# Optimization experiments

Hardware: AMD Instinct MI355X
Metric: run time of the kernel (lower is better)

## Reference

```python
import jax, jax.numpy as jnp
import numpy as np

N = 100000      # nodes_num
E = 1600000     # edges (avg degree 16)
D_IN = 256
D_OUT = 128
EPS = 1e-3      # keras BatchNormalization default epsilon
LEAKY = 0.2     # tf.nn.leaky_relu default alpha


def setup_inputs() -> dict:
    key = jax.random.key(0)
    ks = jax.random.split(key, 6)
    x = jax.random.normal(ks[0], (N, D_IN), jnp.float32)
    w = jax.random.normal(ks[1], (D_IN, D_OUT), jnp.float32) / np.float32(np.sqrt(D_IN))
    w1 = jax.random.normal(ks[2], (D_IN, D_IN), jnp.float32) / np.float32(np.sqrt(D_IN))
    w2 = jax.random.normal(ks[3], (D_IN, D_IN), jnp.float32) / np.float32(np.sqrt(D_IN))
    rows = jnp.sort(jax.random.randint(ks[4], (E,), 0, N, jnp.int32))
    cols = jax.random.randint(ks[5], (E,), 0, N, jnp.int32)
    edge_vals = jnp.ones((E,), jnp.float32)
    return {"x": x, "w": w, "w1": w1, "w2": w2,
            "edge_vals": edge_vals, "rows": rows, "cols": cols}


def reference(x, w, w1, w2, edge_vals, rows, cols):
    # Batch norm (training mode: per-feature stats over node axis, gamma=1, beta=0)
    mean = jnp.mean(x, axis=0)
    var = jnp.var(x, axis=0)
    xn = (x - mean) * jax.lax.rsqrt(var + EPS)          # [N, D_IN]

    mapped = xn @ w                                      # [N, D_OUT]
    s1 = jnp.tanh(jnp.sum((xn @ w1) * xn, axis=1))       # [N] row score
    s2 = jnp.tanh(jnp.sum((xn @ w2) * xn, axis=1))       # [N] col score

    # sparse add of adj*s1[row] and adj*s2[col], then leaky_relu on edge values
    ev = edge_vals * (s1[rows] + s2[cols])               # [E]
    ev = jnp.where(ev > 0, ev, LEAKY * ev)

    # tf.sparse.softmax: softmax over the nonzero entries of each row
    m = jax.ops.segment_max(ev, rows, num_segments=N)    # [N]
    m = jnp.where(jnp.isfinite(m), m, 0.0)               # empty rows -> 0
    ex = jnp.exp(ev - m[rows])
    denom = jax.ops.segment_sum(ex, rows, num_segments=N)
    alpha = ex / denom[rows]                             # [E] edge softmax

    # SpMM: out[i] = sum_{e: rows[e]==i} alpha[e] * mapped[cols[e]]
    out = jax.ops.segment_sum(alpha[:, None] * mapped[cols], rows, num_segments=N)
    return out  # activation is identity (activation=None)
```

## Files before the change

### kernel.cpp

```cpp
#include <hip/hip_runtime.h>

#define D_IN 256
#define D_OUT 128
#define EPS_BN 1e-3f
#define LEAKY 0.2f

typedef unsigned short u16;
typedef unsigned int u32;
typedef u16 u16x4 __attribute__((ext_vector_type(4)));
typedef u16 u16x8 __attribute__((ext_vector_type(8)));
typedef __bf16 bf16x8 __attribute__((ext_vector_type(8)));
typedef float f32x4 __attribute__((ext_vector_type(4)));

__device__ __forceinline__ float bf2f(u16 u) {
    u32 v = ((u32)u) << 16;
    return __uint_as_float(v);
}
__device__ __forceinline__ u16 f2bf(float f) {
    u32 u = __float_as_uint(f);
    u32 r = (u + 0x7FFFu + ((u >> 16) & 1u)) >> 16;
    return (u16)r;
}

__global__ void colstats_k(const float* __restrict__ x, int n,
                           float* __restrict__ sums, float* __restrict__ sqs) {
    int c = threadIdx.x;
    float s = 0.f, q = 0.f;
    for (int r = blockIdx.x; r < n; r += gridDim.x) {
        float v = x[(size_t)r * D_IN + c];
        s += v;
        q += v * v;
    }
    atomicAdd(&sums[c], s);
    atomicAdd(&sqs[c], q);
}

__global__ void finalize_k(const float* __restrict__ sums, const float* __restrict__ sqs,
                           int n, float* __restrict__ mean, float* __restrict__ inv) {
    int c = threadIdx.x;
    float m = sums[c] / (float)n;
    float v = sqs[c] / (float)n - m * m;
    mean[c] = m;
    inv[c] = rsqrtf(v + EPS_BN);
}

__global__ void prep_w_k(const float* __restrict__ w1, const float* __restrict__ w2,
                         const float* __restrict__ w, u16* __restrict__ Bth,
                         u16* __restrict__ Btl, u16* __restrict__ Wth,
                         u16* __restrict__ Wtl) {
    int idx = blockIdx.x * 256 + threadIdx.x;
    int k = idx & 255;
    int nn = idx >> 8;
    if (nn < 512) {
        float v = (nn < 256) ? w1[(size_t)k * 256 + nn]
                             : w2[(size_t)k * 256 + (nn - 256)];
        u16 h = f2bf(v);
        u16 l = f2bf(v - bf2f(h));
        Bth[(size_t)nn * 256 + k] = h;
        Btl[(size_t)nn * 256 + k] = l;
    } else {
        int nm = nn - 512;
        float v = w[(size_t)k * D_OUT + nm];
        u16 h = f2bf(v);
        u16 l = f2bf(v - bf2f(h));
        Wth[(size_t)nm * 256 + k] = h;
        Wtl[(size_t)nm * 256 + k] = l;
    }
}

__device__ __forceinline__ int kmap(int v, int g, int j) {
    return (v == 0) ? (8 * g + j) : (16 * (j >> 2) + 4 * g + (j & 3));
}

__global__ void probe_k(int* __restrict__ flagp) {
    __shared__ float Ar[16][32];
    __shared__ float Br[32][16];
    __shared__ float Dr[16][16];
    int l = threadIdx.x;
    for (int i = l; i < 512; i += 64) {
        int r = i >> 5, k = i & 31;
        Ar[r][k] = (float)(((r * 5 + k * 3) % 11) - 5);
    }
    for (int i = l; i < 512; i += 64) {
        int k = i >> 4, c = i & 15;
        Br[k][c] = (float)(((k * 3 + c * 7) % 13) - 6);
    }
    __syncthreads();
    for (int i = l; i < 256; i += 64) {
        int r = i >> 4, c = i & 15;
        float s = 0.f;
        for (int k = 0; k < 32; ++k) s += Ar[r][k] * Br[k][c];
        Dr[r][c] = s;
    }
    __syncthreads();
    int g = l >> 4, c15 = l & 15;
    int found = -1;
    for (int combo = 0; combo < 4; ++combo) {
        int va = combo >> 1, vb = combo & 1;
        u16x8 af, bfv;
#pragma unroll
        for (int j = 0; j < 8; ++j) {
            af[j] = f2bf(Ar[c15][kmap(va, g, j)]);
            bfv[j] = f2bf(Br[kmap(vb, g, j)][c15]);
        }
        f32x4 d = {0.f, 0.f, 0.f, 0.f};
        d = __builtin_amdgcn_mfma_f32_16x16x32_bf16(
            __builtin_bit_cast(bf16x8, af), __builtin_bit_cast(bf16x8, bfv), d,
            0, 0, 0);
        bool ok = true;
#pragma unroll
        for (int r = 0; r < 4; ++r) ok = ok && (d[r] == Dr[g * 4 + r][c15]);
        if (found < 0 && __all(ok)) found = combo;
    }
    if (l == 0) flagp[0] = (found < 0) ? 0 : found;
}

__device__ __forceinline__ void stage_A(const float* __restrict__ x,
                                        const float* __restrict__ mean,
                                        const float* __restrict__ inv, int m0,
                                        int n, u16* Ah, u16* Al) {
    const int tid = threadIdx.x;
    for (int i = 0; i < 16; ++i) {
        int chunk = tid + (i << 8);
        int r = chunk >> 6;
        int c4 = (chunk & 63) << 2;
        int gr = m0 + r;
        bool ok = gr < n;
        float4 v = make_float4(0.f, 0.f, 0.f, 0.f);
        if (ok) v = *(const float4*)(x + (size_t)gr * D_IN + c4);
        float4 mn = *(const float4*)(mean + c4);
        float4 iv = *(const float4*)(inv + c4);
        float a0 = ok ? (v.x - mn.x) * iv.x : 0.f;
        float a1 = ok ? (v.y - mn.y) * iv.y : 0.f;
        float a2 = ok ? (v.z - mn.z) * iv.z : 0.f;
        float a3 = ok ? (v.w - mn.w) * iv.w : 0.f;
        u16 h0 = f2bf(a0), h1 = f2bf(a1), h2 = f2bf(a2), h3 = f2bf(a3);
        u16 l0 = f2bf(a0 - bf2f(h0)), l1 = f2bf(a1 - bf2f(h1));
        u16 l2 = f2bf(a2 - bf2f(h2)), l3 = f2bf(a3 - bf2f(h3));
        int off = (r << 9) + (((c4 << 1) ^ ((r & 7) << 4)));
        u16x4 hv = {h0, h1, h2, h3};
        u16x4 lv = {l0, l1, l2, l3};
        *(u16x4*)((char*)Ah + off) = hv;
        *(u16x4*)((char*)Al + off) = lv;
    }
}

__device__ __forceinline__ void stage_B(const u16* __restrict__ Gh,
                                        const u16* __restrict__ Gl, int n0,
                                        int k0, u16* Bh, u16* Bl) {
    const int tid = threadIdx.x;
    for (int i = 0; i < 2; ++i) {
        int chunk = tid + (i << 8);
        int nl = chunk >> 3;
        int k8 = (chunk & 7) << 3;
        size_t goff = (size_t)(n0 + nl) * 256 + k0 + k8;
        u16x8 hv = *(const u16x8*)(Gh + goff);
        u16x8 lv = *(const u16x8*)(Gl + goff);
        int off = (nl << 7) + (((k8 << 1) ^ ((nl & 7) << 4)));
        *(u16x8*)((char*)Bh + off) = hv;
        *(u16x8*)((char*)Bl + off) = lv;
    }
}

template <int V>
__device__ __forceinline__ bf16x8 ld_frag(const u16* plane, int rowByteBase,
                                          int swz, int kbyte, int g) {
    const char* p = (const char*)plane + rowByteBase;
    if constexpr (V == 0) {
        u16x8 v = *(const u16x8*)(p + ((kbyte + (g << 4)) ^ swz));
        return __builtin_bit_cast(bf16x8, v);
    } else {
        u16x4 a = *(const u16x4*)(p + ((kbyte + (g << 3)) ^ swz));
        u16x4 b = *(const u16x4*)(p + ((kbyte + 32 + (g << 3)) ^ swz));
        u16x8 v;
        v[0] = a[0]; v[1] = a[1]; v[2] = a[2]; v[3] = a[3];
        v[4] = b[0]; v[5] = b[1]; v[6] = b[2]; v[7] = b[3];
        return __builtin_bit_cast(bf16x8, v);
    }
}

template <int VA, int VB>
__device__ __forceinline__ void quadmap_body(
    const float* __restrict__ x, const u16* __restrict__ Bth,
    const u16* __restrict__ Btl, const u16* __restrict__ Wth,
    const u16* __restrict__ Wtl, const float* __restrict__ mean,
    const float* __restrict__ inv, float* __restrict__ s1,
    float* __restrict__ s2, u16* __restrict__ mapped, int n, int mapCT,
    u16* Ah, u16* Al, u16* Bh, u16* Bl) {
    const int tid = threadIdx.x;
    const int lane = tid & 63, wave = tid >> 6;
    const int g = lane >> 4, c15 = lane & 15;
    const int wm = wave >> 1, wn = wave & 1;
    const int m0 = blockIdx.x * 64;

    stage_A(x, mean, inv, m0, n, Ah, Al);
    __syncthreads();

    float sp[2][4] = {{0.f, 0.f, 0.f, 0.f}, {0.f, 0.f, 0.f, 0.f}};

    for (int jt = 0; jt < 8; ++jt) {
        f32x4 acc[2][2];
#pragma unroll
        for (int mf = 0; mf < 2; ++mf)
#pragma unroll
            for (int nf = 0; nf < 2; ++nf) acc[mf][nf] = (f32x4){0.f, 0.f, 0.f, 0.f};

        for (int kt = 0; kt < 4; ++kt) {
            __syncthreads();
            stage_B(Bth, Btl, jt * 64, kt * 64, Bh, Bl);
            __syncthreads();
#pragma unroll
            for (int kk = 0; kk < 2; ++kk) {
                int kbA = kt * 128 + kk * 64;
                int kbB = kk * 64;
                bf16x8 ah[2], alf[2], bhf[2], blf[2];
#pragma unroll
                for (int mf = 0; mf < 2; ++mf) {
                    int row = wm * 32 + mf * 16 + c15;
                    int swz = (row & 7) << 4;
                    ah[mf] = ld_frag<VA>(Ah, row << 9, swz, kbA, g);
                    alf[mf] = ld_frag<VA>(Al, row << 9, swz, kbA, g);
                }
#pragma unroll
                for (int nf = 0; nf < 2; ++nf) {
                    int nl = wn * 32 + nf * 16 + c15;
                    int swz = (nl & 7) << 4;
                    bhf[nf] = ld_frag<VB>(Bh, nl << 7, swz, kbB, g);
                    blf[nf] = ld_frag<VB>(Bl, nl << 7, swz, kbB, g);
                }
#pragma unroll
                for (int mf = 0; mf < 2; ++mf)
#pragma unroll
                    for (int nf = 0; nf < 2; ++nf) {
                        acc[mf][nf] = __builtin_amdgcn_mfma_f32_16x16x32_bf16(
                            ah[mf], bhf[nf], acc[mf][nf], 0, 0, 0);
                        acc[mf][nf] = __builtin_amdgcn_mfma_f32_16x16x32_bf16(
                            ah[mf], blf[nf], acc[mf][nf], 0, 0, 0);
                        acc[mf][nf] = __builtin_amdgcn_mfma_f32_16x16x32_bf16(
                            alf[mf], bhf[nf], acc[mf][nf], 0, 0, 0);
                    }
            }
        }
        int fcol0 = (jt & 3) << 6;
#pragma unroll
        for (int mf = 0; mf < 2; ++mf) {
#pragma unroll
            for (int nf = 0; nf < 2; ++nf) {
                int col = fcol0 + wn * 32 + nf * 16 + c15;
                float mn = mean[col], ivv = inv[col];
#pragma unroll
                for (int r = 0; r < 4; ++r) {
                    int grow = m0 + wm * 32 + mf * 16 + g * 4 + r;
                    float xv = 0.f;
                    if (grow < n) xv = (x[(size_t)grow * D_IN + col] - mn) * ivv;
                    sp[mf][r] = fmaf(acc[mf][nf][r], xv, sp[mf][r]);
                }
            }
        }
        if ((jt & 3) == 3) {
            float part[2][4];
#pragma unroll
            for (int mf = 0; mf < 2; ++mf)
#pragma unroll
                for (int r = 0; r < 4; ++r) {
                    float v = sp[mf][r];
                    v += __shfl_xor(v, 1);
                    v += __shfl_xor(v, 2);
                    v += __shfl_xor(v, 4);
                    v += __shfl_xor(v, 8);
                    part[mf][r] = v;
                    sp[mf][r] = 0.f;
                }
            float* scratch = (float*)Bh;
            __syncthreads();
            if (c15 == 0) {
#pragma unroll
                for (int mf = 0; mf < 2; ++mf)
#pragma unroll
                    for (int r = 0; r < 4; ++r) {
                        int sidx = (((((wm << 2) | g) << 1) | mf) << 3) | (r << 1) | wn;
                        scratch[sidx] = part[mf][r];
                    }
            }
            __syncthreads();
            if (wn == 0 && c15 == 0) {
                float* dst = (jt < 4) ? s1 : s2;
#pragma unroll
                for (int mf = 0; mf < 2; ++mf)
#pragma unroll
                    for (int r = 0; r < 4; ++r) {
                        int sidx = (((((wm << 2) | g) << 1) | mf) << 3) | (r << 1);
                        float tot = scratch[sidx] + scratch[sidx | 1];
                        int grow = m0 + wm * 32 + mf * 16 + g * 4 + r;
                        if (grow < n) dst[grow] = tanhf(tot);
                    }
            }
            __syncthreads();
        }
    }

    const int tiles = mapCT >> 6;
    for (int t = 0; t < tiles; ++t) {
        f32x4 acc[2][2];
#pragma unroll
        for (int mf = 0; mf < 2; ++mf)
#pragma unroll
            for (int nf = 0; nf < 2; ++nf) acc[mf][nf] = (f32x4){0.f, 0.f, 0.f, 0.f};

        for (int kt = 0; kt < 4; ++kt) {
            __syncthreads();
            stage_B(Wth, Wtl, t * 64, kt * 64, Bh, Bl);
            __syncthreads();
#pragma unroll
            for (int kk = 0; kk < 2; ++kk) {
                int kbA = kt * 128 + kk * 64;
                int kbB = kk * 64;
                bf16x8 ah[2], alf[2], bhf[2], blf[2];
#pragma unroll
                for (int mf = 0; mf < 2; ++mf) {
                    int row = wm * 32 + mf * 16 + c15;
                    int swz = (row & 7) << 4;
                    ah[mf] = ld_frag<VA>(Ah, row << 9, swz, kbA, g);
                    alf[mf] = ld_frag<VA>(Al, row << 9, swz, kbA, g);
                }
#pragma unroll
                for (int nf = 0; nf < 2; ++nf) {
                    int nl = wn * 32 + nf * 16 + c15;
                    int swz = (nl & 7) << 4;
                    bhf[nf] = ld_frag<VB>(Bh, nl << 7, swz, kbB, g);
                    blf[nf] = ld_frag<VB>(Bl, nl << 7, swz, kbB, g);
                }
#pragma unroll
                for (int mf = 0; mf < 2; ++mf)
#pragma unroll
                    for (int nf = 0; nf < 2; ++nf) {
                        acc[mf][nf] = __builtin_amdgcn_mfma_f32_16x16x32_bf16(
                            ah[mf], bhf[nf], acc[mf][nf], 0, 0, 0);
                        acc[mf][nf] = __builtin_amdgcn_mfma_f32_16x16x32_bf16(
                            ah[mf], blf[nf], acc[mf][nf], 0, 0, 0);
                        acc[mf][nf] = __builtin_amdgcn_mfma_f32_16x16x32_bf16(
                            alf[mf], bhf[nf], acc[mf][nf], 0, 0, 0);
                    }
            }
        }
#pragma unroll
        for (int mf = 0; mf < 2; ++mf)
#pragma unroll
            for (int nf = 0; nf < 2; ++nf) {
                int si = t * 64 + wn * 32 + nf * 16 + c15;
#pragma unroll
                for (int r = 0; r < 4; ++r) {
                    int grow = m0 + wm * 32 + mf * 16 + g * 4 + r;
                    if (grow < n)
                        mapped[(size_t)grow * mapCT + si] = f2bf(acc[mf][nf][r]);
                }
            }
    }
}

__global__ __launch_bounds__(256) void quadmap_mfma_k(
    const float* __restrict__ x, const u16* __restrict__ Bth,
    const u16* __restrict__ Btl, const u16* __restrict__ Wth,
    const u16* __restrict__ Wtl, const float* __restrict__ mean,
    const float* __restrict__ inv, float* __restrict__ s1,
    float* __restrict__ s2, u16* __restrict__ mapped,
    const int* __restrict__ flagp, int n, int mapCT) {
    __shared__ u16 Ah[64 * 256];
    __shared__ u16 Al[64 * 256];
    __shared__ u16 Bh[64 * 64];
    __shared__ u16 Bl[64 * 64];
    int v = flagp[0];
    if (v == 1)
        quadmap_body<0, 1>(x, Bth, Btl, Wth, Wtl, mean, inv, s1, s2, mapped, n, mapCT, Ah, Al, Bh, Bl);
    else if (v == 2)
        quadmap_body<1, 0>(x, Bth, Btl, Wth, Wtl, mean, inv, s1, s2, mapped, n, mapCT, Ah, Al, Bh, Bl);
    else if (v == 3)
        quadmap_body<1, 1>(x, Bth, Btl, Wth, Wtl, mean, inv, s1, s2, mapped, n, mapCT, Ah, Al, Bh, Bl);
    else
        quadmap_body<0, 0>(x, Bth, Btl, Wth, Wtl, mean, inv, s1, s2, mapped, n, mapCT, Ah, Al, Bh, Bl);
}

template <int VA, int VB>
__device__ __forceinline__ void map_body(
    const float* __restrict__ x, const u16* __restrict__ Wth,
    const u16* __restrict__ Wtl, const float* __restrict__ mean,
    const float* __restrict__ inv, u16* __restrict__ mapped, int n, int c0,
    int CT, u16* Ah, u16* Al, u16* Bh, u16* Bl) {
    const int tid = threadIdx.x;
    const int lane = tid & 63, wave = tid >> 6;
    const int g = lane >> 4, c15 = lane & 15;
    const int wm = wave >> 1, wn = wave & 1;
    const int m0 = blockIdx.x * 64;

    stage_A(x, mean, inv, m0, n, Ah, Al);
    __syncthreads();

    const int tiles = CT >> 6;
    for (int t = 0; t < tiles; ++t) {
        f32x4 acc[2][2];
#pragma unroll
        for (int mf = 0; mf < 2; ++mf)
#pragma unroll
            for (int nf = 0; nf < 2; ++nf) acc[mf][nf] = (f32x4){0.f, 0.f, 0.f, 0.f};

        for (int kt = 0; kt < 4; ++kt) {
            __syncthreads();
            stage_B(Wth, Wtl, c0 + t * 64, kt * 64, Bh, Bl);
            __syncthreads();
#pragma unroll
            for (int kk = 0; kk < 2; ++kk) {
                int kbA = kt * 128 + kk * 64;
                int kbB = kk * 64;
                bf16x8 ah[2], alf[2], bhf[2], blf[2];
#pragma unroll
                for (int mf = 0; mf < 2; ++mf) {
                    int row = wm * 32 + mf * 16 + c15;
                    int swz = (row & 7) << 4;
                    ah[mf] = ld_frag<VA>(Ah, row << 9, swz, kbA, g);
                    alf[mf] = ld_frag<VA>(Al, row << 9, swz, kbA, g);
                }
#pragma unroll
                for (int nf = 0; nf < 2; ++nf) {
                    int nl = wn * 32 + nf * 16 + c15;
                    int swz = (nl & 7) << 4;
                    bhf[nf] = ld_frag<VB>(Bh, nl << 7, swz, kbB, g);
                    blf[nf] = ld_frag<VB>(Bl, nl << 7, swz, kbB, g);
                }
#pragma unroll
                for (int mf = 0; mf < 2; ++mf)
#pragma unroll
                    for (int nf = 0; nf < 2; ++nf) {
                        acc[mf][nf] = __builtin_amdgcn_mfma_f32_16x16x32_bf16(
                            ah[mf], bhf[nf], acc[mf][nf], 0, 0, 0);
                        acc[mf][nf] = __builtin_amdgcn_mfma_f32_16x16x32_bf16(
                            ah[mf], blf[nf], acc[mf][nf], 0, 0, 0);
                        acc[mf][nf] = __builtin_amdgcn_mfma_f32_16x16x32_bf16(
                            alf[mf], bhf[nf], acc[mf][nf], 0, 0, 0);
                    }
            }
        }
#pragma unroll
        for (int mf = 0; mf < 2; ++mf)
#pragma unroll
            for (int nf = 0; nf < 2; ++nf) {
                int si = t * 64 + wn * 32 + nf * 16 + c15;
#pragma unroll
                for (int r = 0; r < 4; ++r) {
                    int grow = m0 + wm * 32 + mf * 16 + g * 4 + r;
                    if (grow < n) mapped[(size_t)grow * CT + si] = f2bf(acc[mf][nf][r]);
                }
            }
    }
}

__global__ __launch_bounds__(256) void map_mfma_k(
    const float* __restrict__ x, const u16* __restrict__ Wth,
    const u16* __restrict__ Wtl, const float* __restrict__ mean,
    const float* __restrict__ inv, u16* __restrict__ mapped, int n, int c0,
    int CT, const int* __restrict__ flagp) {
    __shared__ u16 Ah[64 * 256];
    __shared__ u16 Al[64 * 256];
    __shared__ u16 Bh[64 * 64];
    __shared__ u16 Bl[64 * 64];
    int v = flagp[0];
    if (v == 1) map_body<0, 1>(x, Wth, Wtl, mean, inv, mapped, n, c0, CT, Ah, Al, Bh, Bl);
    else if (v == 2) map_body<1, 0>(x, Wth, Wtl, mean, inv, mapped, n, c0, CT, Ah, Al, Bh, Bl);
    else if (v == 3) map_body<1, 1>(x, Wth, Wtl, mean, inv, mapped, n, c0, CT, Ah, Al, Bh, Bl);
    else map_body<0, 0>(x, Wth, Wtl, mean, inv, mapped, n, c0, CT, Ah, Al, Bh, Bl);
}

template <typename OT>
__global__ __launch_bounds__(256) void gemm_map_k(const float* __restrict__ x,
                                                  const float* __restrict__ w,
                                                  const float* __restrict__ mean,
                                                  const float* __restrict__ inv,
                                                  OT* __restrict__ outp, int n,
                                                  int c0, int CT) {
    __shared__ float As[64][68];
    __shared__ float Bs[64][68];
    const int tid = threadIdx.x;
    const int tx = tid & 15, ty = tid >> 4;
    const int m0 = blockIdx.x * 64;
    const int tiles = (CT + 63) >> 6;

    for (int t = 0; t < tiles; ++t) {
        const int jt = c0 + (t << 6);
        float acc[4][4];
#pragma unroll
        for (int a = 0; a < 4; ++a)
#pragma unroll
            for (int b = 0; b < 4; ++b) acc[a][b] = 0.f;

        for (int kt = 0; kt < D_IN; kt += 64) {
#pragma unroll
            for (int i = 0; i < 4; ++i) {
                int f4 = tid + 256 * i;
                int r = f4 >> 4;
                int c4 = (f4 & 15) << 2;
                float4 o;
                int gr = m0 + r;
                if (gr < n) {
                    float4 v = *(const float4*)(x + (size_t)gr * D_IN + kt + c4);
                    float4 mn = *(const float4*)(mean + kt + c4);
                    float4 iv = *(const float4*)(inv + kt + c4);
                    o.x = (v.x - mn.x) * iv.x;
                    o.y = (v.y - mn.y) * iv.y;
                    o.z = (v.z - mn.z) * iv.z;
                    o.w = (v.w - mn.w) * iv.w;
                } else {
                    o = make_float4(0.f, 0.f, 0.f, 0.f);
                }
                *(float4*)&As[r][c4] = o;
            }
#pragma unroll
            for (int i = 0; i < 4; ++i) {
                int f4 = tid + 256 * i;
                int r = f4 >> 4;
                int c4 = (f4 & 15) << 2;
                int jc = jt + c4;
                float4 bv = (jc < D_OUT)
                                ? *(const float4*)(w + (size_t)(kt + r) * D_OUT + jc)
                                : make_float4(0.f, 0.f, 0.f, 0.f);
                *(float4*)&Bs[r][c4] = bv;
            }
            __syncthreads();
#pragma unroll 8
            for (int k = 0; k < 64; ++k) {
                float4 bv = *(const float4*)&Bs[k][tx << 2];
                float a0 = As[(ty << 2) + 0][k];
                float a1 = As[(ty << 2) + 1][k];
                float a2 = As[(ty << 2) + 2][k];
                float a3 = As[(ty << 2) + 3][k];
                acc[0][0] = fmaf(a0, bv.x, acc[0][0]);
                acc[0][1] = fmaf(a0, bv.y, acc[0][1]);
                acc[0][2] = fmaf(a0, bv.z, acc[0][2]);
                acc[0][3] = fmaf(a0, bv.w, acc[0][3]);
                acc[1][0] = fmaf(a1, bv.x, acc[1][0]);
                acc[1][1] = fmaf(a1, bv.y, acc[1][1]);
                acc[1][2] = fmaf(a1, bv.z, acc[1][2]);
                acc[1][3] = fmaf(a1, bv.w, acc[1][3]);
                acc[2][0] = fmaf(a2, bv.x, acc[2][0]);
                acc[2][1] = fmaf(a2, bv.y, acc[2][1]);
                acc[2][2] = fmaf(a2, bv.z, acc[2][2]);
                acc[2][3] = fmaf(a2, bv.w, acc[2][3]);
                acc[3][0] = fmaf(a3, bv.x, acc[3][0]);
                acc[3][1] = fmaf(a3, bv.y, acc[3][1]);
                acc[3][2] = fmaf(a3, bv.z, acc[3][2]);
                acc[3][3] = fmaf(a3, bv.w, acc[3][3]);
            }
            __syncthreads();
        }
        int si = (jt - c0) + (tx << 2);
        if (si < CT) {
#pragma unroll
            for (int a = 0; a < 4; ++a) {
                int gm = m0 + (ty << 2) + a;
                if (gm < n) {
                    ushort4 pk;
                    pk.x = f2bf(acc[a][0]);
                    pk.y = f2bf(acc[a][1]);
                    pk.z = f2bf(acc[a][2]);
                    pk.w = f2bf(acc[a][3]);
                    *(ushort4*)((u16*)outp + (size_t)gm * CT + si) = pk;
                }
            }
        }
    }
}

__global__ void build_rowptr_k(const int* __restrict__ rows, int E, int n,
                               int* __restrict__ rp) {
    int e = blockIdx.x * blockDim.x + threadIdx.x;
    if (e >= E) return;
    int r = rows[e];
    int prev = (e == 0) ? -1 : rows[e - 1];
    for (int q = prev + 1; q <= r; ++q) rp[q] = e;
    if (e == E - 1) {
        for (int q = r + 1; q <= n; ++q) rp[q] = E;
    }
}

template <bool WRITE_ALPHA>
__global__ __launch_bounds__(256) void row_softmax_k(
    const int* __restrict__ row_ptr, const int* __restrict__ cols,
    const float* __restrict__ ev, const float* __restrict__ s1,
    const float* __restrict__ s2, float* __restrict__ rmax,
    float* __restrict__ rsm, float* __restrict__ alpha, int n) {
    int wave = threadIdx.x >> 6;
    int lane = threadIdx.x & 63;
    int row = blockIdx.x * 4 + wave;
    if (row >= n) return;
    int e0 = row_ptr[row], e1 = row_ptr[row + 1];
    if (e0 >= e1) {
        if (lane == 0) {
            rmax[row] = 0.f;
            rsm[row] = 0.f;
        }
        return;
    }
    float s1r = s1[row];
    float mx = -1e30f;
    for (int e = e0 + lane; e < e1; e += 64) {
        float v = ev[e] * (s1r + s2[cols[e]]);
        v = v > 0.f ? v : LEAKY * v;
        mx = fmaxf(mx, v);
    }
#pragma unroll
    for (int off = 32; off; off >>= 1) mx = fmaxf(mx, __shfl_xor(mx, off));
    float sm = 0.f;
    for (int e = e0 + lane; e < e1; e += 64) {
        float v = ev[e] * (s1r + s2[cols[e]]);
        v = v > 0.f ? v : LEAKY * v;
        sm += __expf(v - mx);
    }
#pragma unroll
    for (int off = 32; off; off >>= 1) sm += __shfl_xor(sm, off);
    float rsm_v = 1.f / sm;
    if (lane == 0) {
        rmax[row] = mx;
        rsm[row] = rsm_v;
    }
    if constexpr (WRITE_ALPHA) {
        for (int e = e0 + lane; e < e1; e += 64) {
            float v = ev[e] * (s1r + s2[cols[e]]);
            v = v > 0.f ? v : LEAKY * v;
            alpha[e] = __expf(v - mx) * rsm_v;
        }
    }
}

template <bool HAS_ALPHA>
__global__ __launch_bounds__(256) void attn_gather2_k(
    const int* __restrict__ row_ptr, const int* __restrict__ cols,
    const float* __restrict__ alpha, const float* __restrict__ ev,
    const float* __restrict__ s1, const float* __restrict__ s2,
    const float* __restrict__ rmax, const float* __restrict__ rsm,
    const u16* __restrict__ mapped, float* __restrict__ outp, int n, int c0,
    int CT) {
    const int wave = threadIdx.x >> 6;
    const int lane = threadIdx.x & 63;
    const int row = blockIdx.x * 4 + wave;
    if (row >= n) return;
    const int e0 = row_ptr[row], e1 = row_ptr[row + 1];
    float* orow = outp + (size_t)row * D_OUT + c0;
    const int nu = CT >> 1;
    const bool act = lane < nu;
    if (e0 >= e1) {
        if (act) *(float2*)(orow + (lane << 1)) = make_float2(0.f, 0.f);
        return;
    }
    float s1r = 0.f, mxv = 0.f, rsv = 0.f;
    if constexpr (!HAS_ALPHA) {
        s1r = s1[row];
        mxv = rmax[row];
        rsv = rsm[row];
    }
    const u32* map32 = (const u32*)mapped;
    float ox = 0.f, oy = 0.f;
    int e = e0;
    while (e < e1) {
        int cnt = min(e1 - e, 64);
        int ce = 0;
        float ae = 0.f;
        if (lane < cnt) {
            int ee = e + lane;
            ce = cols[ee];
            if constexpr (HAS_ALPHA) {
                ae = alpha[ee];
            } else {
                float v = ev[ee] * (s1r + s2[ce]);
                v = v > 0.f ? v : LEAKY * v;
                ae = __expf(v - mxv) * rsv;
            }
        }
        for (int j0 = 0; j0 < cnt; j0 += 8) {
            int cv[8];
            float av[8];
            u32 mv[8];
#pragma unroll
            for (int j = 0; j < 8; ++j) {
                cv[j] = __shfl(ce, j0 + j);
                av[j] = __shfl(ae, j0 + j);
            }
#pragma unroll
            for (int j = 0; j < 8; ++j)
                mv[j] = act ? map32[(size_t)cv[j] * nu + lane] : 0u;
#pragma unroll
            for (int j = 0; j < 8; ++j) {
                ox = fmaf(av[j], bf2f((u16)(mv[j] & 0xffffu)), ox);
                oy = fmaf(av[j], bf2f((u16)(mv[j] >> 16)), oy);
            }
        }
        e += cnt;
    }
    if (act) *(float2*)(orow + (lane << 1)) = make_float2(ox, oy);
}

extern "C" void kernel_launch(void* const* d_in, const int* in_sizes, int n_in,
                              void* d_out, int out_size, void* d_ws, size_t ws_size,
                              hipStream_t stream) {
    const float* x  = (const float*)d_in[0];
    const float* w  = (const float*)d_in[1];
    const float* w1 = (const float*)d_in[2];
    const float* w2 = (const float*)d_in[3];
    const float* ev = (const float*)d_in[4];
    const int* rows = (const int*)d_in[5];
    const int* cols = (const int*)d_in[6];
    float* out = (float*)d_out;

    const int N = in_sizes[0] / D_IN;
    const int E = in_sizes[4];

    char* base = (char*)d_ws;
    size_t off = 0;
    auto alloc = [&](size_t bytes) -> char* {
        off = (off + 255) & ~(size_t)255;
        char* p = base + off;
        off += bytes;
        return p;
    };
    float* sums  = (float*)alloc(256 * 4);
    float* sqs   = (float*)alloc(256 * 4);
    float* mean  = (float*)alloc(256 * 4);
    float* inv   = (float*)alloc(256 * 4);
    float* s1    = (float*)alloc((size_t)N * 4);
    float* s2    = (float*)alloc((size_t)N * 4);
    float* rmax  = (float*)alloc((size_t)N * 4);
    float* rsm   = (float*)alloc((size_t)N * 4);
    int* row_ptr = (int*)alloc((size_t)(N + 1) * 4);
    int* flag    = (int*)alloc(256);
    u16* Bth = (u16*)alloc((size_t)512 * 256 * 2);
    u16* Btl = (u16*)alloc((size_t)512 * 256 * 2);
    u16* Wth = (u16*)alloc((size_t)128 * 256 * 2);
    u16* Wtl = (u16*)alloc((size_t)128 * 256 * 2);
    size_t head0 = off;

    size_t alpha_bytes = (size_t)E * 4;
    auto fits_alpha = [&](size_t mapped_bytes) {
        size_t o = (head0 + 255) & ~(size_t)255;
        o += alpha_bytes;
        o = (o + 255) & ~(size_t)255;
        return o + mapped_bytes <= ws_size;
    };
    auto fits_noalpha = [&](size_t mapped_bytes) {
        size_t o = (head0 + 255) & ~(size_t)255;
        return o + mapped_bytes <= ws_size;
    };

    bool has_alpha;
    int CT;
    if (fits_alpha((size_t)N * 128 * 2)) {
        has_alpha = true; CT = 128;
    } else if (fits_alpha((size_t)N * 64 * 2)) {
        has_alpha = true; CT = 64;
    } else if (fits_noalpha((size_t)N * 32 * 2)) {
        has_alpha = false; CT = 32;
    } else if (fits_noalpha((size_t)N * 16 * 2)) {
        has_alpha = false; CT = 16;
    } else {
        has_alpha = false; CT = 8;
    }
    float* alpha = has_alpha ? (float*)alloc(alpha_bytes) : nullptr;
    u16* mapped = (u16*)alloc((size_t)N * CT * 2);

    hipMemsetAsync(sums, 0, 512 * sizeof(float), stream);
    colstats_k<<<512, 256, 0, stream>>>(x, N, sums, sqs);
    finalize_k<<<1, 256, 0, stream>>>(sums, sqs, N, mean, inv);
    prep_w_k<<<640, 256, 0, stream>>>(w1, w2, w, Bth, Btl, Wth, Wtl);
    probe_k<<<1, 64, 0, stream>>>(flag);

    int qb = (N + 63) / 64;
// ... 35 lines not shown
```

Measured before the change: 605.3 us.

## Load B fragments directly from global into registers with double-buffered prefetch

Removes the LDS staging of the weight (B) tiles and the two barriers per k-step in the quadratic-score and mapping MFMA kernels. Each wave now reads its B fragments straight from global/L2 into registers, prefetching the next k-slice (and the next tile's first slice) while computing the current one. LDS use drops to the A planes plus a small reduction buffer, and launch bounds ask for two blocks per CU. The cost is more register pressure and redundant global reads of B across waves, which rely on cache hits.

```diff
diff --git a/kernel.cpp b/kernel.cpp
--- a/kernel.cpp
+++ b/kernel.cpp
@@ -145,23 +145,6 @@
     }
 }
 
-__device__ __forceinline__ void stage_B(const u16* __restrict__ Gh,
-                                        const u16* __restrict__ Gl, int n0,
-                                        int k0, u16* Bh, u16* Bl) {
-    const int tid = threadIdx.x;
-    for (int i = 0; i < 2; ++i) {
-        int chunk = tid + (i << 8);
-        int nl = chunk >> 3;
-        int k8 = (chunk & 7) << 3;
-        size_t goff = (size_t)(n0 + nl) * 256 + k0 + k8;
-        u16x8 hv = *(const u16x8*)(Gh + goff);
-        u16x8 lv = *(const u16x8*)(Gl + goff);
-        int off = (nl << 7) + (((k8 << 1) ^ ((nl & 7) << 4)));
-        *(u16x8*)((char*)Bh + off) = hv;
-        *(u16x8*)((char*)Bl + off) = lv;
-    }
-}
-
 template <int V>
 __device__ __forceinline__ bf16x8 ld_frag(const u16* plane, int rowByteBase,
                                           int swz, int kbyte, int g) {
@@ -179,6 +162,85 @@
     }
 }
 
+template <int V>
+__device__ __forceinline__ bf16x8 ld_bg(const u16* __restrict__ G, int nrow,
+                                        int kbyte, int g) {
+    const char* p = (const char*)G + ((size_t)nrow << 9) + kbyte;
+    if constexpr (V == 0) {
+        u16x8 v = *(const u16x8*)(p + (g << 4));
+        return __builtin_bit_cast(bf16x8, v);
+    } else {
+        u16x4 a = *(const u16x4*)(p + (g << 3));
+        u16x4 b = *(const u16x4*)(p + 32 + (g << 3));
+        u16x8 v;
+        v[0] = a[0]; v[1] = a[1]; v[2] = a[2]; v[3] = a[3];
+        v[4] = b[0]; v[5] = b[1]; v[6] = b[2]; v[7] = b[3];
+        return __builtin_bit_cast(bf16x8, v);
+    }
+}
+
+template <int VB_, int PAR>
+__device__ __forceinline__ void pref_b(const u16* __restrict__ Gh,
+                                       const u16* __restrict__ Gl, int nbase,
+                                       int kt, int c15, int g,
+                                       bf16x8 (&pbh)[2][2][2],
+                                       bf16x8 (&pbl)[2][2][2]) {
+#pragma unroll
+    for (int nf = 0; nf < 2; ++nf) {
+        int nrow = nbase + nf * 16 + c15;
+#pragma unroll
+        for (int kk = 0; kk < 2; ++kk) {
+            pbh[PAR][nf][kk] = ld_bg<VB_>(Gh, nrow, kt * 128 + kk * 64, g);
+            pbl[PAR][nf][kk] = ld_bg<VB_>(Gl, nrow, kt * 128 + kk * 64, g);
+        }
+    }
+}
+
+template <int VA_, int PAR, int KK>
+__device__ __forceinline__ void comp_q(const u16* Ah, const u16* Al, int rowb0,
+                                       int rowb1, int swz, int kbA, int g,
+                                       const bf16x8 (&pbh)[2][2][2],
+                                       const bf16x8 (&pbl)[2][2][2],
+                                       f32x4 (&acc)[2][2]) {
+    bf16x8 ah[2], al[2];
+    ah[0] = ld_frag<VA_>(Ah, rowb0, swz, kbA, g);
+    al[0] = ld_frag<VA_>(Al, rowb0, swz, kbA, g);
+    ah[1] = ld_frag<VA_>(Ah, rowb1, swz, kbA, g);
+    al[1] = ld_frag<VA_>(Al, rowb1, swz, kbA, g);
+#pragma unroll
+    for (int mf = 0; mf < 2; ++mf)
+#pragma unroll
+        for (int nf = 0; nf < 2; ++nf) {
+            acc[mf][nf] = __builtin_amdgcn_mfma_f32_16x16x32_bf16(
+                ah[mf], pbh[PAR][nf][KK], acc[mf][nf], 0, 0, 0);
+            acc[mf][nf] = __builtin_amdgcn_mfma_f32_16x16x32_bf16(
+                ah[mf], pbl[PAR][nf][KK], acc[mf][nf], 0, 0, 0);
+            acc[mf][nf] = __builtin_amdgcn_mfma_f32_16x16x32_bf16(
+                al[mf], pbh[PAR][nf][KK], acc[mf][nf], 0, 0, 0);
+        }
+}
+
+template <int VA, int VB>
+__device__ __forceinline__ void tile_mm(
+    const u16* Ah, const u16* Al, const u16* __restrict__ Gh,
+    const u16* __restrict__ Gl, int nbase, const u16* __restrict__ nGh,
+    const u16* __restrict__ nGl, int nnb, int rowb0, int rowb1, int swz,
+    int c15, int g, bf16x8 (&pbh)[2][2][2], bf16x8 (&pbl)[2][2][2],
+    f32x4 (&acc)[2][2]) {
+    pref_b<VB, 1>(Gh, Gl, nbase, 1, c15, g, pbh, pbl);
+    comp_q<VA, 0, 0>(Ah, Al, rowb0, rowb1, swz, 0, g, pbh, pbl, acc);
+    comp_q<VA, 0, 1>(Ah, Al, rowb0, rowb1, swz, 64, g, pbh, pbl, acc);
+    pref_b<VB, 0>(Gh, Gl, nbase, 2, c15, g, pbh, pbl);
+    comp_q<VA, 1, 0>(Ah, Al, rowb0, rowb1, swz, 128, g, pbh, pbl, acc);
+    comp_q<VA, 1, 1>(Ah, Al, rowb0, rowb1, swz, 192, g, pbh, pbl, acc);
+    pref_b<VB, 1>(Gh, Gl, nbase, 3, c15, g, pbh, pbl);
+    comp_q<VA, 0, 0>(Ah, Al, rowb0, rowb1, swz, 256, g, pbh, pbl, acc);
+    comp_q<VA, 0, 1>(Ah, Al, rowb0, rowb1, swz, 320, g, pbh, pbl, acc);
+    pref_b<VB, 0>(nGh, nGl, nnb, 0, c15, g, pbh, pbl);
+    comp_q<VA, 1, 0>(Ah, Al, rowb0, rowb1, swz, 384, g, pbh, pbl, acc);
+    comp_q<VA, 1, 1>(Ah, Al, rowb0, rowb1, swz, 448, g, pbh, pbl, acc);
+}
+
 template <int VA, int VB>
 __device__ __forceinline__ void quadmap_body(
     const float* __restrict__ x, const u16* __restrict__ Bth,
@@ -186,7 +248,7 @@
     const u16* __restrict__ Wtl, const float* __restrict__ mean,
     const float* __restrict__ inv, float* __restrict__ s1,
     float* __restrict__ s2, u16* __restrict__ mapped, int n, int mapCT,
-    u16* Ah, u16* Al, u16* Bh, u16* Bl) {
+    u16* Ah, u16* Al, float* red) {
     const int tid = threadIdx.x;
     const int lane = tid & 63, wave = tid >> 6;
     const int g = lane >> 4, c15 = lane & 15;
@@ -196,51 +258,31 @@
     stage_A(x, mean, inv, m0, n, Ah, Al);
     __syncthreads();
 
+    const int rowb0 = (wm * 32 + c15) << 9;
+    const int rowb1 = (wm * 32 + 16 + c15) << 9;
+    const int swz = (c15 & 7) << 4;
+
+    bf16x8 pbh[2][2][2], pbl[2][2][2];
     float sp[2][4] = {{0.f, 0.f, 0.f, 0.f}, {0.f, 0.f, 0.f, 0.f}};
 
+    pref_b<VB, 0>(Bth, Btl, wn * 32, 0, c15, g, pbh, pbl);
+
     for (int jt = 0; jt < 8; ++jt) {
+        const int nbase = jt * 64 + wn * 32;
         f32x4 acc[2][2];
 #pragma unroll
         for (int mf = 0; mf < 2; ++mf)
 #pragma unroll
             for (int nf = 0; nf < 2; ++nf) acc[mf][nf] = (f32x4){0.f, 0.f, 0.f, 0.f};
 
-        for (int kt = 0; kt < 4; ++kt) {
-            __syncthreads();
-            stage_B(Bth, Btl, jt * 64, kt * 64, Bh, Bl);
-            __syncthreads();
-#pragma unroll
-            for (int kk = 0; kk < 2; ++kk) {
-                int kbA = kt * 128 + kk * 64;
-                int kbB = kk * 64;
-                bf16x8 ah[2], alf[2], bhf[2], blf[2];
-#pragma unroll
-                for (int mf = 0; mf < 2; ++mf) {
-                    int row = wm * 32 + mf * 16 + c15;
-                    int swz = (row & 7) << 4;
-                    ah[mf] = ld_frag<VA>(Ah, row << 9, swz, kbA, g);
-                    alf[mf] = ld_frag<VA>(Al, row << 9, swz, kbA, g);
-                }
-#pragma unroll
-                for (int nf = 0; nf < 2; ++nf) {
-                    int nl = wn * 32 + nf * 16 + c15;
-                    int swz = (nl & 7) << 4;
-                    bhf[nf] = ld_frag<VB>(Bh, nl << 7, swz, kbB, g);
-                    blf[nf] = ld_frag<VB>(Bl, nl << 7, swz, kbB, g);
-                }
-#pragma unroll
-                for (int mf = 0; mf < 2; ++mf)
-#pragma unroll
-                    for (int nf = 0; nf < 2; ++nf) {
-                        acc[mf][nf] = __builtin_amdgcn_mfma_f32_16x16x32_bf16(
-                            ah[mf], bhf[nf], acc[mf][nf], 0, 0, 0);
-                        acc[mf][nf] = __builtin_amdgcn_mfma_f32_16x16x32_bf16(
-                            ah[mf], blf[nf], acc[mf][nf], 0, 0, 0);
-                        acc[mf][nf] = __builtin_amdgcn_mfma_f32_16x16x32_bf16(
-                            alf[mf], bhf[nf], acc[mf][nf], 0, 0, 0);
-                    }
-            }
-        }
+        const u16 *nGh, *nGl;
+        int nnb;
+        if (jt < 7) { nGh = Bth; nGl = Btl; nnb = nbase + 64; }
+        else        { nGh = Wth; nGl = Wtl; nnb = wn * 32; }
+
+        tile_mm<VA, VB>(Ah, Al, Bth, Btl, nbase, nGh, nGl, nnb, rowb0, rowb1,
+                        swz, c15, g, pbh, pbl, acc);
+
         int fcol0 = (jt & 3) << 6;
 #pragma unroll
         for (int mf = 0; mf < 2; ++mf) {
@@ -271,7 +313,6 @@
                     part[mf][r] = v;
                     sp[mf][r] = 0.f;
                 }
-            float* scratch = (float*)Bh;
             __syncthreads();
             if (c15 == 0) {
 #pragma unroll
@@ -279,7 +320,7 @@
 #pragma unroll
                     for (int r = 0; r < 4; ++r) {
                         int sidx = (((((wm << 2) | g) << 1) | mf) << 3) | (r << 1) | wn;
-                        scratch[sidx] = part[mf][r];
+                        red[sidx] = part[mf][r];
                     }
             }
             __syncthreads();
@@ -290,7 +331,7 @@
 #pragma unroll
                     for (int r = 0; r < 4; ++r) {
                         int sidx = (((((wm << 2) | g) << 1) | mf) << 3) | (r << 1);
-                        float tot = scratch[sidx] + scratch[sidx | 1];
+                        float tot = red[sidx] + red[sidx | 1];
                         int grow = m0 + wm * 32 + mf * 16 + g * 4 + r;
                         if (grow < n) dst[grow] = tanhf(tot);
                     }
@@ -301,48 +342,17 @@
 
     const int tiles = mapCT >> 6;
     for (int t = 0; t < tiles; ++t) {
+        const int nbase = t * 64 + wn * 32;
+        const int nnb = ((t + 1 < tiles) ? (t + 1) * 64 : 0) + wn * 32;
         f32x4 acc[2][2];
 #pragma unroll
         for (int mf = 0; mf < 2; ++mf)
 #pragma unroll
             for (int nf = 0; nf < 2; ++nf) acc[mf][nf] = (f32x4){0.f, 0.f, 0.f, 0.f};
 
-        for (int kt = 0; kt < 4; ++kt) {
-            __syncthreads();
-            stage_B(Wth, Wtl, t * 64, kt * 64, Bh, Bl);
-            __syncthreads();
-#pragma unroll
-            for (int kk = 0; kk < 2; ++kk) {
-                int kbA = kt * 128 + kk * 64;
-                int kbB = kk * 64;
-                bf16x8 ah[2], alf[2], bhf[2], blf[2];
-#pragma unroll
-                for (int mf = 0; mf < 2; ++mf) {
-                    int row = wm * 32 + mf * 16 + c15;
-                    int swz = (row & 7) << 4;
-                    ah[mf] = ld_frag<VA>(Ah, row << 9, swz, kbA, g);
-                    alf[mf] = ld_frag<VA>(Al, row << 9, swz, kbA, g);
-                }
-#pragma unroll
-                for (int nf = 0; nf < 2; ++nf) {
-                    int nl = wn * 32 + nf * 16 + c15;
-                    int swz = (nl & 7) << 4;
-                    bhf[nf] = ld_frag<VB>(Bh, nl << 7, swz, kbB, g);
-                    blf[nf] = ld_frag<VB>(Bl, nl << 7, swz, kbB, g);
-                }
-#pragma unroll
-                for (int mf = 0; mf < 2; ++mf)
-#pragma unroll
-                    for (int nf = 0; nf < 2; ++nf) {
-                        acc[mf][nf] = __builtin_amdgcn_mfma_f32_16x16x32_bf16(
-                            ah[mf], bhf[nf], acc[mf][nf], 0, 0, 0);
-                        acc[mf][nf] = __builtin_amdgcn_mfma_f32_16x16x32_bf16(
-                            ah[mf], blf[nf], acc[mf][nf], 0, 0, 0);
-                        acc[mf][nf] = __builtin_amdgcn_mfma_f32_16x16x32_bf16(
-                            alf[mf], bhf[nf], acc[mf][nf], 0, 0, 0);
-                    }
-            }
-        }
+        tile_mm<VA, VB>(Ah, Al, Wth, Wtl, nbase, Wth, Wtl, nnb, rowb0, rowb1,
+                        swz, c15, g, pbh, pbl, acc);
+
 #pragma unroll
         for (int mf = 0; mf < 2; ++mf)
 #pragma unroll
@@ -358,7 +368,7 @@
     }
 }
 
-__global__ __launch_bounds__(256) void quadmap_mfma_k(
+__global__ __launch_bounds__(256, 2) void quadmap_mfma_k(
     const float* __restrict__ x, const u16* __restrict__ Bth,
     const u16* __restrict__ Btl, const u16* __restrict__ Wth,
     const u16* __restrict__ Wtl, const float* __restrict__ mean,
@@ -367,17 +377,16 @@
     const int* __restrict__ flagp, int n, int mapCT) {
     __shared__ u16 Ah[64 * 256];
     __shared__ u16 Al[64 * 256];
-    __shared__ u16 Bh[64 * 64];
-    __shared__ u16 Bl[64 * 64];
+    __shared__ float red[128];
     int v = flagp[0];
     if (v == 1)
-        quadmap_body<0, 1>(x, Bth, Btl, Wth, Wtl, mean, inv, s1, s2, mapped, n, mapCT, Ah, Al, Bh, Bl);
+        quadmap_body<0, 1>(x, Bth, Btl, Wth, Wtl, mean, inv, s1, s2, mapped, n, mapCT, Ah, Al, red);
     else if (v == 2)
-        quadmap_body<1, 0>(x, Bth, Btl, Wth, Wtl, mean, inv, s1, s2, mapped, n, mapCT, Ah, Al, Bh, Bl);
+        quadmap_body<1, 0>(x, Bth, Btl, Wth, Wtl, mean, inv, s1, s2, mapped, n, mapCT, Ah, Al, red);
     else if (v == 3)
-        quadmap_body<1, 1>(x, Bth, Btl, Wth, Wtl, mean, inv, s1, s2, mapped, n, mapCT, Ah, Al, Bh, Bl);
+        quadmap_body<1, 1>(x, Bth, Btl, Wth, Wtl, mean, inv, s1, s2, mapped, n, mapCT, Ah, Al, red);
     else
-        quadmap_body<0, 0>(x, Bth, Btl, Wth, Wtl, mean, inv, s1, s2, mapped, n, mapCT, Ah, Al, Bh, Bl);
+        quadmap_body<0, 0>(x, Bth, Btl, Wth, Wtl, mean, inv, s1, s2, mapped, n, mapCT, Ah, Al, red);
 }
 
 template <int VA, int VB>
@@ -385,7 +394,7 @@
     const float* __restrict__ x, const u16* __restrict__ Wth,
     const u16* __restrict__ Wtl, const float* __restrict__ mean,
     const float* __restrict__ inv, u16* __restrict__ mapped, int n, int c0,
-    int CT, u16* Ah, u16* Al, u16* Bh, u16* Bl) {
+    int CT, u16* Ah, u16* Al) {
     const int tid = threadIdx.x;
     const int lane = tid & 63, wave = tid >> 6;
     const int g = lane >> 4, c15 = lane & 15;
@@ -395,50 +404,26 @@
     stage_A(x, mean, inv, m0, n, Ah, Al);
     __syncthreads();
 
+    const int rowb0 = (wm * 32 + c15) << 9;
+    const int rowb1 = (wm * 32 + 16 + c15) << 9;
+    const int swz = (c15 & 7) << 4;
+
+    bf16x8 pbh[2][2][2], pbl[2][2][2];
+    pref_b<VB, 0>(Wth, Wtl, c0 + wn * 32, 0, c15, g, pbh, pbl);
+
     const int tiles = CT >> 6;
     for (int t = 0; t < tiles; ++t) {
+        const int nbase = c0 + t * 64 + wn * 32;
+        const int nnb = c0 + ((t + 1 < tiles) ? (t + 1) * 64 : 0) + wn * 32;
         f32x4 acc[2][2];
 #pragma unroll
         for (int mf = 0; mf < 2; ++mf)
 #pragma unroll
             for (int nf = 0; nf < 2; ++nf) acc[mf][nf] = (f32x4){0.f, 0.f, 0.f, 0.f};
 
-        for (int kt = 0; kt < 4; ++kt) {
-            __syncthreads();
-            stage_B(Wth, Wtl, c0 + t * 64, kt * 64, Bh, Bl);
-            __syncthreads();
-#pragma unroll
-            for (int kk = 0; kk < 2; ++kk) {
-                int kbA = kt * 128 + kk * 64;
-                int kbB = kk * 64;
-                bf16x8 ah[2], alf[2], bhf[2], blf[2];
-#pragma unroll
-                for (int mf = 0; mf < 2; ++mf) {
-                    int row = wm * 32 + mf * 16 + c15;
-                    int swz = (row & 7) << 4;
-                    ah[mf] = ld_frag<VA>(Ah, row << 9, swz, kbA, g);
-                    alf[mf] = ld_frag<VA>(Al, row << 9, swz, kbA, g);
-                }
-#pragma unroll
-                for (int nf = 0; nf < 2; ++nf) {
-                    int nl = wn * 32 + nf * 16 + c15;
-                    int swz = (nl & 7) << 4;
-                    bhf[nf] = ld_frag<VB>(Bh, nl << 7, swz, kbB, g);
-                    blf[nf] = ld_frag<VB>(Bl, nl << 7, swz, kbB, g);
-                }
-#pragma unroll
-                for (int mf = 0; mf < 2; ++mf)
-#pragma unroll
-                    for (int nf = 0; nf < 2; ++nf) {
-                        acc[mf][nf] = __builtin_amdgcn_mfma_f32_16x16x32_bf16(
-                            ah[mf], bhf[nf], acc[mf][nf], 0, 0, 0);
-                        acc[mf][nf] = __builtin_amdgcn_mfma_f32_16x16x32_bf16(
-                            ah[mf], blf[nf], acc[mf][nf], 0, 0, 0);
-                        acc[mf][nf] = __builtin_amdgcn_mfma_f32_16x16x32_bf16(
-                            alf[mf], bhf[nf], acc[mf][nf], 0, 0, 0);
-                    }
-            }
-        }
+        tile_mm<VA, VB>(Ah, Al, Wth, Wtl, nbase, Wth, Wtl, nnb, rowb0, rowb1,
+                        swz, c15, g, pbh, pbl, acc);
+
 #pragma unroll
         for (int mf = 0; mf < 2; ++mf)
 #pragma unroll
@@ -453,20 +438,18 @@
     }
 }
 
-__global__ __launch_bounds__(256) void map_mfma_k(
+__global__ __launch_bounds__(256, 2) void map_mfma_k(
     const float* __restrict__ x, const u16* __restrict__ Wth,
     const u16* __restrict__ Wtl, const float* __restrict__ mean,
     const float* __restrict__ inv, u16* __restrict__ mapped, int n, int c0,
     int CT, const int* __restrict__ flagp) {
     __shared__ u16 Ah[64 * 256];
     __shared__ u16 Al[64 * 256];
-    __shared__ u16 Bh[64 * 64];
-    __shared__ u16 Bl[64 * 64];
     int v = flagp[0];
-    if (v == 1) map_body<0, 1>(x, Wth, Wtl, mean, inv, mapped, n, c0, CT, Ah, Al, Bh, Bl);
-    else if (v == 2) map_body<1, 0>(x, Wth, Wtl, mean, inv, mapped, n, c0, CT, Ah, Al, Bh, Bl);
-    else if (v == 3) map_body<1, 1>(x, Wth, Wtl, mean, inv, mapped, n, c0, CT, Ah, Al, Bh, Bl);
-    else map_body<0, 0>(x, Wth, Wtl, mean, inv, mapped, n, c0, CT, Ah, Al, Bh, Bl);
+    if (v == 1) map_body<0, 1>(x, Wth, Wtl, mean, inv, mapped, n, c0, CT, Ah, Al);
+    else if (v == 2) map_body<1, 0>(x, Wth, Wtl, mean, inv, mapped, n, c0, CT, Ah, Al);
+    else if (v == 3) map_body<1, 1>(x, Wth, Wtl, mean, inv, mapped, n, c0, CT, Ah, Al);
+    else map_body<0, 0>(x, Wth, Wtl, mean, inv, mapped, n, c0, CT, Ah, Al);
 }
 
 template <typename OT>
```

Measured after the change: 740.8 us. 1.22x slower.

## Prefetch next B tile into registers and use LDS-only barriers in MFMA GEMMs

Applied to the files above, without the earlier changes.

The B-tile staging in the quadmap and map GEMM kernels is split into a global-to-register load and a register-to-LDS store. The next tile's global load is issued before the compute on the current tile, so global latency overlaps the MFMA work. __syncthreads is replaced with a barrier that waits only on LDS counters (lgkmcnt), so in-flight global loads do not stall it, and one redundant barrier after the score reduction is dropped. This adds register pressure and relies on the hand-placed waitcnt to keep LDS reuse correct, particularly the scratch buffer that aliases Bh.

```diff
diff --git a/kernel.cpp b/kernel.cpp
--- a/kernel.cpp
+++ b/kernel.cpp
@@ -20,6 +20,12 @@
     u32 u = __float_as_uint(f);
     u32 r = (u + 0x7FFFu + ((u >> 16) & 1u)) >> 16;
     return (u16)r;
+}
+
+__device__ __forceinline__ void bar_lgkm() {
+    asm volatile("s_waitcnt lgkmcnt(0)" ::: "memory");
+    __builtin_amdgcn_s_barrier();
+    asm volatile("" ::: "memory");
 }
 
 __global__ void colstats_k(const float* __restrict__ x, int n,
@@ -145,20 +151,31 @@
     }
 }
 
-__device__ __forceinline__ void stage_B(const u16* __restrict__ Gh,
-                                        const u16* __restrict__ Gl, int n0,
-                                        int k0, u16* Bh, u16* Bl) {
-    const int tid = threadIdx.x;
+__device__ __forceinline__ void ldb_regs(const u16* __restrict__ Gh,
+                                         const u16* __restrict__ Gl, int n0,
+                                         int k0, int tid, u16x8 (&hv)[2],
+                                         u16x8 (&lv)[2]) {
+#pragma unroll
     for (int i = 0; i < 2; ++i) {
         int chunk = tid + (i << 8);
         int nl = chunk >> 3;
         int k8 = (chunk & 7) << 3;
         size_t goff = (size_t)(n0 + nl) * 256 + k0 + k8;
-        u16x8 hv = *(const u16x8*)(Gh + goff);
-        u16x8 lv = *(const u16x8*)(Gl + goff);
+        hv[i] = *(const u16x8*)(Gh + goff);
+        lv[i] = *(const u16x8*)(Gl + goff);
+    }
+}
+__device__ __forceinline__ void stb_lds(u16* Bh, u16* Bl, int tid,
+                                        const u16x8 (&hv)[2],
+                                        const u16x8 (&lv)[2]) {
+#pragma unroll
+    for (int i = 0; i < 2; ++i) {
+        int chunk = tid + (i << 8);
+        int nl = chunk >> 3;
+        int k8 = (chunk & 7) << 3;
         int off = (nl << 7) + (((k8 << 1) ^ ((nl & 7) << 4)));
-        *(u16x8*)((char*)Bh + off) = hv;
-        *(u16x8*)((char*)Bl + off) = lv;
+        *(u16x8*)((char*)Bh + off) = hv[i];
+        *(u16x8*)((char*)Bl + off) = lv[i];
     }
 }
 
@@ -180,6 +197,44 @@
 }
 
 template <int VA, int VB>
+__device__ __forceinline__ void comp_kt(const u16* Ah, const u16* Al,
+                                        const u16* Bh, const u16* Bl, int kt,
+                                        int wm, int wn, int c15, int g,
+                                        f32x4 (&acc)[2][2]) {
+#pragma unroll
+    for (int kk = 0; kk < 2; ++kk) {
+        int kbA = kt * 128 + kk * 64;
+        int kbB = kk * 64;
+        bf16x8 ah[2], alf[2], bhf[2], blf[2];
+#pragma unroll
+        for (int mf = 0; mf < 2; ++mf) {
+            int row = wm * 32 + mf * 16 + c15;
+            int swz = (row & 7) << 4;
+            ah[mf] = ld_frag<VA>(Ah, row << 9, swz, kbA, g);
+            alf[mf] = ld_frag<VA>(Al, row << 9, swz, kbA, g);
+        }
+#pragma unroll
+        for (int nf = 0; nf < 2; ++nf) {
+            int nl = wn * 32 + nf * 16 + c15;
+            int swz = (nl & 7) << 4;
+            bhf[nf] = ld_frag<VB>(Bh, nl << 7, swz, kbB, g);
+            blf[nf] = ld_frag<VB>(Bl, nl << 7, swz, kbB, g);
+        }
+#pragma unroll
+        for (int mf = 0; mf < 2; ++mf)
+#pragma unroll
+            for (int nf = 0; nf < 2; ++nf) {
+                acc[mf][nf] = __builtin_amdgcn_mfma_f32_16x16x32_bf16(
+                    ah[mf], bhf[nf], acc[mf][nf], 0, 0, 0);
+                acc[mf][nf] = __builtin_amdgcn_mfma_f32_16x16x32_bf16(
+                    ah[mf], blf[nf], acc[mf][nf], 0, 0, 0);
+                acc[mf][nf] = __builtin_amdgcn_mfma_f32_16x16x32_bf16(
+                    alf[mf], bhf[nf], acc[mf][nf], 0, 0, 0);
+            }
+    }
+}
+
+template <int VA, int VB>
 __device__ __forceinline__ void quadmap_body(
     const float* __restrict__ x, const u16* __restrict__ Bth,
     const u16* __restrict__ Btl, const u16* __restrict__ Wth,
@@ -196,6 +251,9 @@
     stage_A(x, mean, inv, m0, n, Ah, Al);
     __syncthreads();
 
+    u16x8 rbh[2], rbl[2];
+    ldb_regs(Bth, Btl, 0, 0, tid, rbh, rbl);
+
     float sp[2][4] = {{0.f, 0.f, 0.f, 0.f}, {0.f, 0.f, 0.f, 0.f}};
 
     for (int jt = 0; jt < 8; ++jt) {
@@ -206,41 +264,18 @@
             for (int nf = 0; nf < 2; ++nf) acc[mf][nf] = (f32x4){0.f, 0.f, 0.f, 0.f};
 
         for (int kt = 0; kt < 4; ++kt) {
-            __syncthreads();
-            stage_B(Bth, Btl, jt * 64, kt * 64, Bh, Bl);
-            __syncthreads();
-#pragma unroll
-            for (int kk = 0; kk < 2; ++kk) {
-                int kbA = kt * 128 + kk * 64;
-                int kbB = kk * 64;
-                bf16x8 ah[2], alf[2], bhf[2], blf[2];
-#pragma unroll
-                for (int mf = 0; mf < 2; ++mf) {
-                    int row = wm * 32 + mf * 16 + c15;
-                    int swz = (row & 7) << 4;
-                    ah[mf] = ld_frag<VA>(Ah, row << 9, swz, kbA, g);
-                    alf[mf] = ld_frag<VA>(Al, row << 9, swz, kbA, g);
-                }
-#pragma unroll
-                for (int nf = 0; nf < 2; ++nf) {
-                    int nl = wn * 32 + nf * 16 + c15;
-                    int swz = (nl & 7) << 4;
-                    bhf[nf] = ld_frag<VB>(Bh, nl << 7, swz, kbB, g);
-                    blf[nf] = ld_frag<VB>(Bl, nl << 7, swz, kbB, g);
-                }
-#pragma unroll
-                for (int mf = 0; mf < 2; ++mf)
-#pragma unroll
-                    for (int nf = 0; nf < 2; ++nf) {
-                        acc[mf][nf] = __builtin_amdgcn_mfma_f32_16x16x32_bf16(
-                            ah[mf], bhf[nf], acc[mf][nf], 0, 0, 0);
-                        acc[mf][nf] = __builtin_amdgcn_mfma_f32_16x16x32_bf16(
-                            ah[mf], blf[nf], acc[mf][nf], 0, 0, 0);
-                        acc[mf][nf] = __builtin_amdgcn_mfma_f32_16x16x32_bf16(
-                            alf[mf], bhf[nf], acc[mf][nf], 0, 0, 0);
-                    }
-            }
-        }
+            bar_lgkm();
+            stb_lds(Bh, Bl, tid, rbh, rbl);
+            const u16 *sH, *sL;
+            int nn0, nk0;
+            if (kt < 3)      { sH = Bth; sL = Btl; nn0 = jt * 64;       nk0 = (kt + 1) * 64; }
+            else if (jt < 7) { sH = Bth; sL = Btl; nn0 = (jt + 1) * 64; nk0 = 0; }
+            else             { sH = Wth; sL = Wtl; nn0 = 0;             nk0 = 0; }
+            ldb_regs(sH, sL, nn0, nk0, tid, rbh, rbl);
+            bar_lgkm();
+            comp_kt<VA, VB>(Ah, Al, Bh, Bl, kt, wm, wn, c15, g, acc);
+        }
+
         int fcol0 = (jt & 3) << 6;
 #pragma unroll
         for (int mf = 0; mf < 2; ++mf) {
@@ -272,7 +307,7 @@
                     sp[mf][r] = 0.f;
                 }
             float* scratch = (float*)Bh;
-            __syncthreads();
+            bar_lgkm();
             if (c15 == 0) {
 #pragma unroll
                 for (int mf = 0; mf < 2; ++mf)
@@ -282,7 +317,7 @@
                         scratch[sidx] = part[mf][r];
                     }
             }
-            __syncthreads();
+            bar_lgkm();
             if (wn == 0 && c15 == 0) {
                 float* dst = (jt < 4) ? s1 : s2;
 #pragma unroll
@@ -295,7 +330,6 @@
                         if (grow < n) dst[grow] = tanhf(tot);
                     }
             }
-            __syncthreads();
         }
     }
 
@@ -308,40 +342,13 @@
             for (int nf = 0; nf < 2; ++nf) acc[mf][nf] = (f32x4){0.f, 0.f, 0.f, 0.f};
 
         for (int kt = 0; kt < 4; ++kt) {
-            __syncthreads();
-            stage_B(Wth, Wtl, t * 64, kt * 64, Bh, Bl);
-            __syncthreads();
-#pragma unroll
-            for (int kk = 0; kk < 2; ++kk) {
-                int kbA = kt * 128 + kk * 64;
-                int kbB = kk * 64;
-                bf16x8 ah[2], alf[2], bhf[2], blf[2];
-#pragma unroll
-                for (int mf = 0; mf < 2; ++mf) {
-                    int row = wm * 32 + mf * 16 + c15;
-                    int swz = (row & 7) << 4;
-                    ah[mf] = ld_frag<VA>(Ah, row << 9, swz, kbA, g);
-                    alf[mf] = ld_frag<VA>(Al, row << 9, swz, kbA, g);
-                }
-#pragma unroll
-                for (int nf = 0; nf < 2; ++nf) {
-                    int nl = wn * 32 + nf * 16 + c15;
-                    int swz = (nl & 7) << 4;
-                    bhf[nf] = ld_frag<VB>(Bh, nl << 7, swz, kbB, g);
-                    blf[nf] = ld_frag<VB>(Bl, nl << 7, swz, kbB, g);
-                }
-#pragma unroll
-                for (int mf = 0; mf < 2; ++mf)
-#pragma unroll
-                    for (int nf = 0; nf < 2; ++nf) {
-                        acc[mf][nf] = __builtin_amdgcn_mfma_f32_16x16x32_bf16(
-                            ah[mf], bhf[nf], acc[mf][nf], 0, 0, 0);
-                        acc[mf][nf] = __builtin_amdgcn_mfma_f32_16x16x32_bf16(
-                            ah[mf], blf[nf], acc[mf][nf], 0, 0, 0);
-                        acc[mf][nf] = __builtin_amdgcn_mfma_f32_16x16x32_bf16(
-                            alf[mf], bhf[nf], acc[mf][nf], 0, 0, 0);
-                    }
-            }
+            bar_lgkm();
+            stb_lds(Bh, Bl, tid, rbh, rbl);
+            int nn0 = (kt < 3) ? t * 64 : ((t + 1 < tiles) ? (t + 1) * 64 : t * 64);
+            int nk0 = (kt < 3) ? (kt + 1) * 64 : 0;
+            ldb_regs(Wth, Wtl, nn0, nk0, tid, rbh, rbl);
+            bar_lgkm();
+            comp_kt<VA, VB>(Ah, Al, Bh, Bl, kt, wm, wn, c15, g, acc);
         }
 #pragma unroll
         for (int mf = 0; mf < 2; ++mf)
@@ -395,6 +402,9 @@
     stage_A(x, mean, inv, m0, n, Ah, Al);
     __syncthreads();
 
+    u16x8 rbh[2], rbl[2];
+    ldb_regs(Wth, Wtl, c0, 0, tid, rbh, rbl);
+
     const int tiles = CT >> 6;
     for (int t = 0; t < tiles; ++t) {
         f32x4 acc[2][2];
@@ -404,40 +414,14 @@
             for (int nf = 0; nf < 2; ++nf) acc[mf][nf] = (f32x4){0.f, 0.f, 0.f, 0.f};
 
         for (int kt = 0; kt < 4; ++kt) {
-            __syncthreads();
-            stage_B(Wth, Wtl, c0 + t * 64, kt * 64, Bh, Bl);
-            __syncthreads();
-#pragma unroll
-            for (int kk = 0; kk < 2; ++kk) {
-                int kbA = kt * 128 + kk * 64;
-                int kbB = kk * 64;
-                bf16x8 ah[2], alf[2], bhf[2], blf[2];
-#pragma unroll
-                for (int mf = 0; mf < 2; ++mf) {
-                    int row = wm * 32 + mf * 16 + c15;
-                    int swz = (row & 7) << 4;
-                    ah[mf] = ld_frag<VA>(Ah, row << 9, swz, kbA, g);
-                    alf[mf] = ld_frag<VA>(Al, row << 9, swz, kbA, g);
-                }
-#pragma unroll
-                for (int nf = 0; nf < 2; ++nf) {
-                    int nl = wn * 32 + nf * 16 + c15;
-                    int swz = (nl & 7) << 4;
-                    bhf[nf] = ld_frag<VB>(Bh, nl << 7, swz, kbB, g);
-                    blf[nf] = ld_frag<VB>(Bl, nl << 7, swz, kbB, g);
-                }
-#pragma unroll
-                for (int mf = 0; mf < 2; ++mf)
-#pragma unroll
-                    for (int nf = 0; nf < 2; ++nf) {
-                        acc[mf][nf] = __builtin_amdgcn_mfma_f32_16x16x32_bf16(
-                            ah[mf], bhf[nf], acc[mf][nf], 0, 0, 0);
-                        acc[mf][nf] = __builtin_amdgcn_mfma_f32_16x16x32_bf16(
-                            ah[mf], blf[nf], acc[mf][nf], 0, 0, 0);
-                        acc[mf][nf] = __builtin_amdgcn_mfma_f32_16x16x32_bf16(
-                            alf[mf], bhf[nf], acc[mf][nf], 0, 0, 0);
-                    }
-            }
+            bar_lgkm();
+            stb_lds(Bh, Bl, tid, rbh, rbl);
+            int nn0 = (kt < 3) ? c0 + t * 64
+                               : c0 + ((t + 1 < tiles) ? (t + 1) * 64 : t * 64);
+            int nk0 = (kt < 3) ? (kt + 1) * 64 : 0;
+            ldb_regs(Wth, Wtl, nn0, nk0, tid, rbh, rbl);
+            bar_lgkm();
+            comp_kt<VA, VB>(Ah, Al, Bh, Bl, kt, wm, wn, c15, g, acc);
         }
 #pragma unroll
         for (int mf = 0; mf < 2; ++mf)
```

New measurement: 584.7 us. 3.4% less time.
